# Performance work log

Measured on AMD Instinct MI355X. Metric: run time of the kernel, lower is better.

## Reference

```python
import jax, jax.numpy as jnp
import numpy as np

EPS = 1e-5


def _gcn_norm(edge_index, N):
    # symmetric GCN normalization with self-loops: D^-1/2 (A+I) D^-1/2
    row, col = edge_index[0], edge_index[1]
    loop = jnp.arange(N, dtype=row.dtype)
    row_f = jnp.concatenate([row, loop])
    col_f = jnp.concatenate([col, loop])
    deg = jax.ops.segment_sum(jnp.ones_like(row_f, dtype=jnp.float32), row_f, num_segments=N)
    dinv = jnp.where(deg > 0, jax.lax.rsqrt(jnp.maximum(deg, 1.0)), 0.0)
    norm = dinv[row_f] * dinv[col_f]  # [E+N]
    return row_f, col_f, norm


def _gcn_conv(h, W, b, row_f, col_f, norm, N):
    h = h @ W  # [N, C_out] small GEMM
    msg = h[col_f] * norm[:, None]  # gather over edges  [E+N, C_out]
    return jax.ops.segment_sum(msg, row_f, num_segments=N) + b


def _bn_eval(h, gamma, beta, mean, var):
    return (h - mean) * jax.lax.rsqrt(var + EPS) * gamma + beta


def setup_inputs() -> dict:
    key = jax.random.key(0)
    ks = jax.random.split(key, 12)
    N, E = 100000, 1600000
    C_in, C_hid, C_out = 64, 64, 64
    x = jax.random.normal(ks[0], (N, C_in), dtype=jnp.float32)
    edge_index = jax.random.randint(ks[1], (2, E), 0, N, dtype=jnp.int32)
    s = 1.0 / np.sqrt(C_hid)
    inp = {
        "x": x,
        "edge_index": edge_index,
        "W1": jax.random.normal(ks[2], (C_in, C_hid), dtype=jnp.float32) * s,
        "b1": jnp.zeros((C_hid,), jnp.float32),
        "g1": jnp.ones((C_hid,), jnp.float32),
        "be1": jnp.zeros((C_hid,), jnp.float32),
        "m1": jax.random.normal(ks[3], (C_hid,), dtype=jnp.float32) * 0.1,
        "v1": jax.random.uniform(ks[4], (C_hid,), minval=0.5, maxval=1.5, dtype=jnp.float32),
        "W2": jax.random.normal(ks[5], (C_hid, C_hid), dtype=jnp.float32) * s,
        "b2": jnp.zeros((C_hid,), jnp.float32),
        "g2": jnp.ones((C_hid,), jnp.float32),
        "be2": jnp.zeros((C_hid,), jnp.float32),
        "m2": jax.random.normal(ks[6], (C_hid,), dtype=jnp.float32) * 0.1,
        "v2": jax.random.uniform(ks[7], (C_hid,), minval=0.5, maxval=1.5, dtype=jnp.float32),
        "W3": jax.random.normal(ks[8], (C_hid, C_out), dtype=jnp.float32) * s,
        "b3": jnp.zeros((C_out,), jnp.float32),
    }
    return inp


def reference(x, edge_index, W1, b1, g1, be1, m1, v1, W2, b2, g2, be2, m2, v2, W3, b3):
    N = x.shape[0]
    row_f, col_f, norm = _gcn_norm(edge_index, N)  # cached=True: computed once
    h = _gcn_conv(x, W1, b1, row_f, col_f, norm, N)
    h = jax.nn.relu(_bn_eval(h, g1, be1, m1, v1))  # dropout off (eval)
    h = _gcn_conv(h, W2, b2, row_f, col_f, norm, N)
    h = jax.nn.relu(_bn_eval(h, g2, be2, m2, v2))
    global_embeddings = h
    hc_predictions = _gcn_conv(global_embeddings, W3, b3, row_f, col_f, norm, N)
    return (global_embeddings, hc_predictions)
```

## Files before the change

kernel.cpp:

```cpp
#include <hip/hip_runtime.h>

typedef __attribute__((ext_vector_type(8))) short bfrag8;
typedef __attribute__((ext_vector_type(4))) float facc4;
typedef __attribute__((ext_vector_type(8))) unsigned short u16x8;

#define CROWS  256
#define NCBMAX 512
#define CAP    8192
#define CHUNK  4096
#define SLACK  772
#define BPITCH (CAP + SLACK)

static __device__ __forceinline__ float bf2f(ushort u) {
    union { unsigned int i; float f; } x;
    x.i = ((unsigned int)u) << 16;
    return x.f;
}
static __device__ __forceinline__ ushort f2bf(float f) {
    union { float f; unsigned int i; } x;
    x.f = f;
    unsigned int r = x.i + 0x7FFFu + ((x.i >> 16) & 1u);
    return (ushort)(r >> 16);
}


__global__ void k_cinit(int* __restrict__ ccur, int ncb,
                        ushort* __restrict__ ta, ushort* __restrict__ tb, int N) {
    int b = blockIdx.x * blockDim.x + threadIdx.x;
    if (b < ncb) ccur[b] = b * CAP;
    if (blockIdx.x == 0 && threadIdx.x < 64) {
        ta[(size_t)N * 64 + threadIdx.x] = 0;
        tb[(size_t)N * 64 + threadIdx.x] = 0;
    }
}

__global__ void k_part(const int* __restrict__ row, const int* __restrict__ col, int E,
                       int* __restrict__ ccur, int* __restrict__ bkt, int ncb) {
    __shared__ int recs[CHUNK];
    __shared__ unsigned short cbl[CHUNK];
    __shared__ int hist[NCBMAX], lbase[NCBMAX], loff[NCBMAX];
    int tid = threadIdx.x;
    int chunk0 = blockIdx.x * CHUNK;
    for (int i = tid; i < ncb; i += blockDim.x) hist[i] = 0;
    __syncthreads();
    for (int j = tid; j < CHUNK; j += blockDim.x) {
        int e = chunk0 + j;
        if (e < E) {
            int r = row[e];
            int cb = r >> 8;
            recs[j] = ((r & (CROWS - 1)) << 17) | col[e];
            cbl[j] = (unsigned short)cb;
            atomicAdd(&hist[cb], 1);
        } else cbl[j] = 0xFFFF;
    }
    __syncthreads();
    for (int i = tid; i < ncb; i += blockDim.x) {
        int h = hist[i];
        lbase[i] = h ? atomicAdd(&ccur[i], h) : 0;
        loff[i] = 0;
    }
    __syncthreads();
    for (int j = tid; j < CHUNK; j += blockDim.x) {
        unsigned short cb = cbl[j];
        if (cb != 0xFFFF) {
            int p = lbase[cb] + atomicAdd(&loff[cb], 1);
            if (p < (cb + 1) * CAP) bkt[p] = recs[j];
        }
    }
}

__global__ void k_build(const int* __restrict__ bkt, const int* __restrict__ ccur,
                        int* __restrict__ rptr, int* __restrict__ deg,
                        float* __restrict__ dinv, int* __restrict__ cidx, int N) {
    __shared__ int hist[CROWS], wstart[CROWS], cur[CROWS], psum[CROWS];
    int tid = threadIdx.x;
    int b = blockIdx.x;
    int lo = b * CROWS;
    int nr = min(CROWS, N - lo);
    int in0 = b * CAP;
    int cntE = min(ccur[b] - in0, CAP);
    int out0 = b * BPITCH;

    if (tid < CROWS) hist[tid] = 0;
    __syncthreads();
    for (int i = tid; i < cntE; i += blockDim.x)
        atomicAdd(&hist[bkt[in0 + i] >> 17], 1);
    __syncthreads();
    int d = 0, ep = 0;
    if (tid < CROWS) {
        d = hist[tid];
        ep = (d + 3) & ~3;
        psum[tid] = ep;
    }
    __syncthreads();
    #pragma unroll
    for (int off = 1; off < CROWS; off <<= 1) {
        int t = (tid >= off && tid < CROWS) ? psum[tid - off] : 0;
        __syncthreads();
        if (tid < CROWS) psum[tid] += t;
        __syncthreads();
    }
    if (tid < CROWS) {
        int ws = out0 + psum[tid] - ep;
        wstart[tid] = ws;
        cur[tid] = ws;
        if (tid < nr) {
            rptr[lo + tid] = ws;
            deg[lo + tid] = d;
            dinv[lo + tid] = rsqrtf((float)(d + 1));
        }
    }
    __syncthreads();
    for (int i = tid; i < cntE; i += blockDim.x) {
        int v = bkt[in0 + i];
        int p = atomicAdd(&cur[v >> 17], 1);
        cidx[p] = v & 0x1FFFF;
    }
    __syncthreads();
    if (tid < nr)
        for (int j = d; j < ep; j++) cidx[wstart[tid] + j] = N;
}

template <bool FP32IN>
__global__ void k_gemm(const void* __restrict__ Hv, const float* __restrict__ W,
                       const float* __restrict__ dinv,
                       ushort* __restrict__ T, int ntiles, int N) {
    int lane = threadIdx.x & 63;
    int wid = (blockIdx.x * blockDim.x + threadIdx.x) >> 6;
    int nw = (gridDim.x * blockDim.x) >> 6;
    int m = lane & 15, quad = lane >> 4;

    bfrag8 bf[2][4];
    #pragma unroll
    for (int s = 0; s < 2; s++)
        #pragma unroll
        for (int c = 0; c < 4; c++) {
            bfrag8 f;
            #pragma unroll
            for (int j = 0; j < 8; j++) {
                int k = 32 * s + quad * 8 + j;
                f[j] = (short)f2bf(W[k * 64 + 16 * c + m]);
            }
            bf[s][c] = f;
        }

    for (int t = wid; t < ntiles; t += nw) {
        int nodeA = t * 16 + m;
        if (nodeA >= N) nodeA = N - 1;
        bfrag8 a0, a1;
        if (FP32IN) {
            const float* arow = (const float*)Hv + (size_t)nodeA * 64;
            #pragma unroll
            for (int s = 0; s < 2; s++) {
                float4 u0 = *(const float4*)(arow + s * 32 + quad * 8);
                float4 u1 = *(const float4*)(arow + s * 32 + quad * 8 + 4);
                bfrag8 f;
                f[0] = (short)f2bf(u0.x); f[1] = (short)f2bf(u0.y);
                f[2] = (short)f2bf(u0.z); f[3] = (short)f2bf(u0.w);
                f[4] = (short)f2bf(u1.x); f[5] = (short)f2bf(u1.y);
                f[6] = (short)f2bf(u1.z); f[7] = (short)f2bf(u1.w);
                if (s == 0) a0 = f; else a1 = f;
            }
        } else {
            const ushort* arow = (const ushort*)Hv + (size_t)nodeA * 64;
            a0 = *(const bfrag8*)(arow + quad * 8);
            a1 = *(const bfrag8*)(arow + 32 + quad * 8);
        }
        facc4 acc[4];
        #pragma unroll
        for (int c = 0; c < 4; c++) { acc[c][0]=0.f; acc[c][1]=0.f; acc[c][2]=0.f; acc[c][3]=0.f; }
        #pragma unroll
        for (int c = 0; c < 4; c++) {
            acc[c] = __builtin_amdgcn_mfma_f32_16x16x32_bf16(a0, bf[0][c], acc[c], 0, 0, 0);
            acc[c] = __builtin_amdgcn_mfma_f32_16x16x32_bf16(a1, bf[1][c], acc[c], 0, 0, 0);
        }
        #pragma unroll
        for (int c = 0; c < 4; c++)
            #pragma unroll
            for (int r = 0; r < 4; r++) {
                int node = t * 16 + quad * 4 + r;
                if (node < N)
                    T[(size_t)node * 64 + c * 16 + m] = f2bf(dinv[node] * acc[c][r]);
            }
    }
}

template <bool FUSE>
__global__ void k_aggf(const ushort* __restrict__ T2, const int* __restrict__ rptr,
                       const int* __restrict__ deg, const float* __restrict__ dinv,
                       const int* __restrict__ cidx,
                       const float* __restrict__ bias, const float* __restrict__ g,
                       const float* __restrict__ be, const float* __restrict__ mm,
                       const float* __restrict__ vv, int do_bn,
                       const float* __restrict__ Wn,
                       float* __restrict__ outf, ushort* __restrict__ Tn, int N) {
    __shared__ ushort lds_h[32][72];

    int tid = threadIdx.x;
    int lane = tid & 63;
    int wl = tid >> 6;
    int grp = lane >> 3;
    int s = lane & 7;
    int loc = wl * 8 + grp;
    int r = blockIdx.x * 32 + loc;
    bool rv = (r < N);

    float bb[8], sc[8], sh[8];
    #pragma unroll
    for (int k = 0; k < 8; k++) { bb[k] = bias[s * 8 + k]; sc[k] = 1.f; sh[k] = 0.f; }
    if (do_bn) {
        #pragma unroll
        for (int k = 0; k < 8; k++) {
            sc[k] = g[s * 8 + k] * rsqrtf(vv[s * 8 + k] + 1e-5f);
            sh[k] = be[s * 8 + k] - mm[s * 8 + k] * sc[k];
        }
    }

    int start = rv ? rptr[r] : 0;
    int ep = rv ? ((deg[r] + 3) & ~3) : 0;
    float a[8];
    #pragma unroll
    for (int k = 0; k < 8; k++) a[k] = 0.f;
    int i = 0;
    for (; i + 8 <= ep; i += 8) {
        int4 c4 = *(const int4*)(cidx + start + i);
        int4 d4 = *(const int4*)(cidx + start + i + 4);
        u16x8 t0 = *(const u16x8*)(T2 + (size_t)c4.x * 64 + s * 8);
        u16x8 t1 = *(const u16x8*)(T2 + (size_t)c4.y * 64 + s * 8);
        u16x8 t2 = *(const u16x8*)(T2 + (size_t)c4.z * 64 + s * 8);
        u16x8 t3 = *(const u16x8*)(T2 + (size_t)c4.w * 64 + s * 8);
        u16x8 t4 = *(const u16x8*)(T2 + (size_t)d4.x * 64 + s * 8);
        u16x8 t5 = *(const u16x8*)(T2 + (size_t)d4.y * 64 + s * 8);
        u16x8 t6 = *(const u16x8*)(T2 + (size_t)d4.z * 64 + s * 8);
        u16x8 t7 = *(const u16x8*)(T2 + (size_t)d4.w * 64 + s * 8);
        #pragma unroll
        for (int k = 0; k < 8; k++)
            a[k] += ((bf2f(t0[k]) + bf2f(t1[k])) + (bf2f(t2[k]) + bf2f(t3[k]))) +
                    ((bf2f(t4[k]) + bf2f(t5[k])) + (bf2f(t6[k]) + bf2f(t7[k])));
    }
    if (i < ep) {
        int4 c4 = *(const int4*)(cidx + start + i);
        u16x8 t0 = *(const u16x8*)(T2 + (size_t)c4.x * 64 + s * 8);
        u16x8 t1 = *(const u16x8*)(T2 + (size_t)c4.y * 64 + s * 8);
        u16x8 t2 = *(const u16x8*)(T2 + (size_t)c4.z * 64 + s * 8);
        u16x8 t3 = *(const u16x8*)(T2 + (size_t)c4.w * 64 + s * 8);
        #pragma unroll
        for (int k = 0; k < 8; k++)
            a[k] += (bf2f(t0[k]) + bf2f(t1[k])) + (bf2f(t2[k]) + bf2f(t3[k]));
    }

    float v[8];
    #pragma unroll
    for (int k = 0; k < 8; k++) v[k] = 0.f;
    if (rv) {
        u16x8 sf = *(const u16x8*)(T2 + (size_t)r * 64 + s * 8);
        float dr = dinv[r];
        #pragma unroll
        for (int k = 0; k < 8; k++) {
            v[k] = dr * (a[k] + bf2f(sf[k])) + bb[k];
            if (do_bn) v[k] = fmaxf(v[k] * sc[k] + sh[k], 0.f);
        }
        if (outf) {
            *(float4*)(outf + (size_t)r * 64 + s * 8) = make_float4(v[0], v[1], v[2], v[3]);
            *(float4*)(outf + (size_t)r * 64 + s * 8 + 4) = make_float4(v[4], v[5], v[6], v[7]);
        }
    }

    if constexpr (FUSE) {
        u16x8 hv;
        #pragma unroll
        for (int k = 0; k < 8; k++) hv[k] = rv ? f2bf(v[k]) : (ushort)0;
        *(u16x8*)&lds_h[loc][s * 8] = hv;

        int m = lane & 15, quad = lane >> 4;
        int rtile = wl >> 1, chalf = wl & 1;
        bfrag8 bw[2][2];
        #pragma unroll
        for (int ks = 0; ks < 2; ks++)
            #pragma unroll
            for (int c = 0; c < 2; c++) {
                bfrag8 f;
                #pragma unroll
                for (int j = 0; j < 8; j++) {
                    int k = 32 * ks + quad * 8 + j;
                    f[j] = (short)f2bf(Wn[k * 64 + chalf * 32 + c * 16 + m]);
                }
                bw[ks][c] = f;
            }
        __syncthreads();

        bfrag8 a0 = *(const bfrag8*)&lds_h[rtile * 16 + m][quad * 8];
        bfrag8 a1 = *(const bfrag8*)&lds_h[rtile * 16 + m][32 + quad * 8];
        facc4 acc[2];
        #pragma unroll
        for (int c = 0; c < 2; c++) { acc[c][0]=0.f; acc[c][1]=0.f; acc[c][2]=0.f; acc[c][3]=0.f; }
        #pragma unroll
        for (int c = 0; c < 2; c++) {
            acc[c] = __builtin_amdgcn_mfma_f32_16x16x32_bf16(a0, bw[0][c], acc[c], 0, 0, 0);
            acc[c] = __builtin_amdgcn_mfma_f32_16x16x32_bf16(a1, bw[1][c], acc[c], 0, 0, 0);
        }
        int nodeBase = blockIdx.x * 32 + rtile * 16;
        #pragma unroll
        for (int c = 0; c < 2; c++)
            #pragma unroll
            for (int rr = 0; rr < 4; rr++) {
                int node = nodeBase + quad * 4 + rr;
                if (node < N)
                    Tn[(size_t)node * 64 + chalf * 32 + c * 16 + m] =
                        f2bf(dinv[node] * acc[c][rr]);
            }
    }
}


extern "C" void kernel_launch(void* const* d_in, const int* in_sizes, int n_in,
                              void* d_out, int out_size, void* d_ws, size_t ws_size,
                              hipStream_t stream) {
    const float* x  = (const float*)d_in[0];
    const int*   ei = (const int*)d_in[1];
    const float *W1 = (const float*)d_in[2],  *b1 = (const float*)d_in[3];
    const float *g1 = (const float*)d_in[4],  *be1= (const float*)d_in[5];
    const float *m1 = (const float*)d_in[6],  *v1 = (const float*)d_in[7];
    const float *W2 = (const float*)d_in[8],  *b2 = (const float*)d_in[9];
    const float *g2 = (const float*)d_in[10], *be2= (const float*)d_in[11];
    const float *m2 = (const float*)d_in[12], *v2 = (const float*)d_in[13];
    const float *W3 = (const float*)d_in[14], *b3 = (const float*)d_in[15];

    int N = in_sizes[0] / 64;
    int E = in_sizes[1] / 2;
    const int* row = ei;
    const int* col = ei + E;
    int ncb = (N + CROWS - 1) / CROWS;

    char* p = (char*)d_ws;
    auto take = [&](size_t b) -> char* {
        char* q = p;
        p += (b + 255) & ~(size_t)255;
        return q;
    };
    int*    ccur  = (int*)   take((size_t)ncb * 4);
    int*    rptr  = (int*)   take((size_t)N * 4);
    int*    deg   = (int*)   take((size_t)N * 4);
    float*  dinv  = (float*) take((size_t)N * 4);
    int*    bkt   = (int*)   take((size_t)ncb * CAP * 4);
    int*    cidx  = (int*)   take((size_t)ncb * BPITCH * 4 + 1024);
    ushort* ta    = (ushort*)take((size_t)(N + 1) * 64 * 2);
    ushort* tb    = (ushort*)take((size_t)(N + 1) * 64 * 2);

    const int TB = 256;
    const int TBP = 1024;
    int nchunks = (E + CHUNK - 1) / CHUNK;
    k_cinit<<<(ncb + TB - 1) / TB, TB, 0, stream>>>(ccur, ncb, ta, tb, N);
    k_part <<<nchunks, TBP, 0, stream>>>(row, col, E, ccur, bkt, ncb);
    k_build<<<ncb, TBP, 0, stream>>>(bkt, ccur, rptr, deg, dinv, cidx, N);

    float* outp = (float*)d_out;
    int ntiles = (N + 15) >> 4;
    int GG = (ntiles + 3) / 4;
    int GA = (N + 31) / 32;

    k_gemm<true><<<GG, TB, 0, stream>>>(x, W1, dinv, ta, ntiles, N);
    k_aggf<true><<<GA, TB, 0, stream>>>(ta, rptr, deg, dinv, cidx, b1, g1, be1, m1, v1, 1,
                                        W2, (float*)nullptr, tb, N);
    k_aggf<true><<<GA, TB, 0, stream>>>(tb, rptr, deg, dinv, cidx, b2, g2, be2, m2, v2, 1,
                                        W3, outp, ta, N);
    k_aggf<false><<<GA, TB, 0, stream>>>(ta, rptr, deg, dinv, cidx, b3, b3, b3, b3, b3, 0,
                                         (const float*)nullptr,
                                         outp + (size_t)N * 64, (ushort*)nullptr, N);
}
```

Before: 272.1 us.

## Sort CSR neighbors by column tile and prepack weights and BN params

The CSR build now histograms edges per (row, column-tile) sub-bucket, so each row's neighbor list is grouped by source-node range. The aim is better cache locality during the gather in the aggregation kernels. A new prep kernel converts the three weight matrices once into a bf16 MFMA-fragment layout and folds bias plus batch-norm into one scale and shift per channel, so every block no longer repeats the strided float-to-bf16 weight loads and rsqrt. The cost is larger LDS histograms in k_build and one extra small kernel launch.

```diff
diff --git a/kernel.cpp b/kernel.cpp
--- a/kernel.cpp
+++ b/kernel.cpp
@@ -10,6 +10,8 @@
 #define CHUNK  4096
 #define SLACK  772
 #define BPITCH (CAP + SLACK)
+#define TSH    14
+#define NTMAX  8
 
 static __device__ __forceinline__ float bf2f(ushort u) {
     union { unsigned int i; float f; } x;
@@ -21,6 +23,41 @@
     x.f = f;
     unsigned int r = x.i + 0x7FFFu + ((x.i >> 16) & 1u);
     return (ushort)(r >> 16);
+}
+
+__global__ void k_prep(const float* __restrict__ W1, const float* __restrict__ W2,
+                       const float* __restrict__ W3,
+                       const float* __restrict__ b1, const float* __restrict__ g1,
+                       const float* __restrict__ be1, const float* __restrict__ m1,
+                       const float* __restrict__ v1,
+                       const float* __restrict__ b2, const float* __restrict__ g2,
+                       const float* __restrict__ be2, const float* __restrict__ m2,
+                       const float* __restrict__ v2,
+                       const float* __restrict__ b3,
+                       ushort* __restrict__ wp, float* __restrict__ pp) {
+    int l = blockIdx.x;
+    const float* W = (l == 0) ? W1 : (l == 1) ? W2 : W3;
+    ushort* wo = wp + l * 4096;
+    for (int idx = threadIdx.x; idx < 4096; idx += blockDim.x) {
+        int j = idx & 7, m = (idx >> 3) & 15, quad = (idx >> 7) & 3;
+        int ks = (idx >> 9) & 1, c2 = idx >> 10;
+        wo[idx] = f2bf(W[(32 * ks + 8 * quad + j) * 64 + c2 * 16 + m]);
+    }
+    if (threadIdx.x < 64) {
+        int ch = threadIdx.x;
+        float PS, PH;
+        if (l == 0) {
+            float sc = g1[ch] * rsqrtf(v1[ch] + 1e-5f);
+            PS = sc; PH = be1[ch] - m1[ch] * sc + b1[ch] * sc;
+        } else if (l == 1) {
+            float sc = g2[ch] * rsqrtf(v2[ch] + 1e-5f);
+            PS = sc; PH = be2[ch] - m2[ch] * sc + b2[ch] * sc;
+        } else {
+            PS = 1.f; PH = b3[ch];
+        }
+        pp[l * 128 + ch] = PS;
+        pp[l * 128 + 64 + ch] = PH;
+    }
 }
 
 
@@ -72,7 +109,9 @@
 __global__ void k_build(const int* __restrict__ bkt, const int* __restrict__ ccur,
                         int* __restrict__ rptr, int* __restrict__ deg,
                         float* __restrict__ dinv, int* __restrict__ cidx, int N) {
-    __shared__ int hist[CROWS], wstart[CROWS], cur[CROWS], psum[CROWS];
+    __shared__ int hist4[CROWS * NTMAX];
+    __shared__ int cur4[CROWS * NTMAX];
+    __shared__ int wstart[CROWS], psum[CROWS], degs[CROWS];
     int tid = threadIdx.x;
     int b = blockIdx.x;
     int lo = b * CROWS;
@@ -81,16 +120,20 @@
     int cntE = min(ccur[b] - in0, CAP);
     int out0 = b * BPITCH;
 
-    if (tid < CROWS) hist[tid] = 0;
-    __syncthreads();
-    for (int i = tid; i < cntE; i += blockDim.x)
-        atomicAdd(&hist[bkt[in0 + i] >> 17], 1);
+    for (int i = tid; i < CROWS * NTMAX; i += blockDim.x) hist4[i] = 0;
+    __syncthreads();
+    for (int i = tid; i < cntE; i += blockDim.x) {
+        int v = bkt[in0 + i];
+        atomicAdd(&hist4[(v >> 17) * NTMAX + ((v & 0x1FFFF) >> TSH)], 1);
+    }
     __syncthreads();
     int d = 0, ep = 0;
     if (tid < CROWS) {
-        d = hist[tid];
+        #pragma unroll
+        for (int t = 0; t < NTMAX; t++) d += hist4[tid * NTMAX + t];
         ep = (d + 3) & ~3;
         psum[tid] = ep;
+        degs[tid] = d;
     }
     __syncthreads();
     #pragma unroll
@@ -103,7 +146,12 @@
     if (tid < CROWS) {
         int ws = out0 + psum[tid] - ep;
         wstart[tid] = ws;
-        cur[tid] = ws;
+        int off = ws;
+        #pragma unroll
+        for (int t = 0; t < NTMAX; t++) {
+            cur4[tid * NTMAX + t] = off;
+            off += hist4[tid * NTMAX + t];
+        }
         if (tid < nr) {
             rptr[lo + tid] = ws;
             deg[lo + tid] = d;
@@ -113,16 +161,19 @@
     __syncthreads();
     for (int i = tid; i < cntE; i += blockDim.x) {
         int v = bkt[in0 + i];
-        int p = atomicAdd(&cur[v >> 17], 1);
-        cidx[p] = v & 0x1FFFF;
-    }
-    __syncthreads();
-    if (tid < nr)
-        for (int j = d; j < ep; j++) cidx[wstart[tid] + j] = N;
-}
-
-template <bool FP32IN>
-__global__ void k_gemm(const void* __restrict__ Hv, const float* __restrict__ W,
+        int c = v & 0x1FFFF;
+        int p = atomicAdd(&cur4[(v >> 17) * NTMAX + (c >> TSH)], 1);
+        cidx[p] = c;
+    }
+    __syncthreads();
+    if (tid < nr) {
+        int dd = degs[tid];
+        int epp = (dd + 3) & ~3;
+        for (int j = dd; j < epp; j++) cidx[wstart[tid] + j] = N;
+    }
+}
+
+__global__ void k_gemm(const float* __restrict__ Hv, const ushort* __restrict__ wq,
                        const float* __restrict__ dinv,
                        ushort* __restrict__ T, int ntiles, int N) {
     int lane = threadIdx.x & 63;
@@ -134,37 +185,25 @@
     #pragma unroll
     for (int s = 0; s < 2; s++)
         #pragma unroll
-        for (int c = 0; c < 4; c++) {
-            bfrag8 f;
-            #pragma unroll
-            for (int j = 0; j < 8; j++) {
-                int k = 32 * s + quad * 8 + j;
-                f[j] = (short)f2bf(W[k * 64 + 16 * c + m]);
-            }
-            bf[s][c] = f;
-        }
+        for (int c = 0; c < 4; c++)
+            bf[s][c] = *(const bfrag8*)(wq +
+                (size_t)((((c * 2 + s) * 4 + quad) * 16 + m) * 8));
 
     for (int t = wid; t < ntiles; t += nw) {
         int nodeA = t * 16 + m;
         if (nodeA >= N) nodeA = N - 1;
         bfrag8 a0, a1;
-        if (FP32IN) {
-            const float* arow = (const float*)Hv + (size_t)nodeA * 64;
-            #pragma unroll
-            for (int s = 0; s < 2; s++) {
-                float4 u0 = *(const float4*)(arow + s * 32 + quad * 8);
-                float4 u1 = *(const float4*)(arow + s * 32 + quad * 8 + 4);
-                bfrag8 f;
-                f[0] = (short)f2bf(u0.x); f[1] = (short)f2bf(u0.y);
-                f[2] = (short)f2bf(u0.z); f[3] = (short)f2bf(u0.w);
-                f[4] = (short)f2bf(u1.x); f[5] = (short)f2bf(u1.y);
-                f[6] = (short)f2bf(u1.z); f[7] = (short)f2bf(u1.w);
-                if (s == 0) a0 = f; else a1 = f;
-            }
-        } else {
-            const ushort* arow = (const ushort*)Hv + (size_t)nodeA * 64;
-            a0 = *(const bfrag8*)(arow + quad * 8);
-            a1 = *(const bfrag8*)(arow + 32 + quad * 8);
+        const float* arow = Hv + (size_t)nodeA * 64;
+        #pragma unroll
+        for (int s = 0; s < 2; s++) {
+            float4 u0 = *(const float4*)(arow + s * 32 + quad * 8);
+            float4 u1 = *(const float4*)(arow + s * 32 + quad * 8 + 4);
+            bfrag8 f;
+            f[0] = (short)f2bf(u0.x); f[1] = (short)f2bf(u0.y);
+            f[2] = (short)f2bf(u0.z); f[3] = (short)f2bf(u0.w);
+            f[4] = (short)f2bf(u1.x); f[5] = (short)f2bf(u1.y);
+            f[6] = (short)f2bf(u1.z); f[7] = (short)f2bf(u1.w);
+            if (s == 0) a0 = f; else a1 = f;
         }
         facc4 acc[4];
         #pragma unroll
@@ -189,10 +228,8 @@
 __global__ void k_aggf(const ushort* __restrict__ T2, const int* __restrict__ rptr,
                        const int* __restrict__ deg, const float* __restrict__ dinv,
                        const int* __restrict__ cidx,
-                       const float* __restrict__ bias, const float* __restrict__ g,
-                       const float* __restrict__ be, const float* __restrict__ mm,
-                       const float* __restrict__ vv, int do_bn,
-                       const float* __restrict__ Wn,
+                       const float* __restrict__ pp, int relu,
+                       const ushort* __restrict__ wq,
                        float* __restrict__ outf, ushort* __restrict__ Tn, int N) {
     __shared__ ushort lds_h[32][72];
 
@@ -204,17 +241,6 @@
     int loc = wl * 8 + grp;
     int r = blockIdx.x * 32 + loc;
     bool rv = (r < N);
-
-    float bb[8], sc[8], sh[8];
-    #pragma unroll
-    for (int k = 0; k < 8; k++) { bb[k] = bias[s * 8 + k]; sc[k] = 1.f; sh[k] = 0.f; }
-    if (do_bn) {
-        #pragma unroll
-        for (int k = 0; k < 8; k++) {
-            sc[k] = g[s * 8 + k] * rsqrtf(vv[s * 8 + k] + 1e-5f);
-            sh[k] = be[s * 8 + k] - mm[s * 8 + k] * sc[k];
-        }
-    }
 
     int start = rv ? rptr[r] : 0;
     int ep = rv ? ((deg[r] + 3) & ~3) : 0;
@@ -249,6 +275,13 @@
             a[k] += (bf2f(t0[k]) + bf2f(t1[k])) + (bf2f(t2[k]) + bf2f(t3[k]));
     }
 
+    float4 ps0 = *(const float4*)(pp + s * 8);
+    float4 ps1 = *(const float4*)(pp + s * 8 + 4);
+    float4 ph0 = *(const float4*)(pp + 64 + s * 8);
+    float4 ph1 = *(const float4*)(pp + 64 + s * 8 + 4);
+    float PS[8] = {ps0.x, ps0.y, ps0.z, ps0.w, ps1.x, ps1.y, ps1.z, ps1.w};
+    float PH[8] = {ph0.x, ph0.y, ph0.z, ph0.w, ph1.x, ph1.y, ph1.z, ph1.w};
+
     float v[8];
     #pragma unroll
     for (int k = 0; k < 8; k++) v[k] = 0.f;
@@ -257,8 +290,8 @@
         float dr = dinv[r];
         #pragma unroll
         for (int k = 0; k < 8; k++) {
-            v[k] = dr * (a[k] + bf2f(sf[k])) + bb[k];
-            if (do_bn) v[k] = fmaxf(v[k] * sc[k] + sh[k], 0.f);
+            v[k] = dr * (a[k] + bf2f(sf[k])) * PS[k] + PH[k];
+            if (relu) v[k] = fmaxf(v[k], 0.f);
         }
         if (outf) {
             *(float4*)(outf + (size_t)r * 64 + s * 8) = make_float4(v[0], v[1], v[2], v[3]);
@@ -278,15 +311,9 @@
         #pragma unroll
         for (int ks = 0; ks < 2; ks++)
             #pragma unroll
-            for (int c = 0; c < 2; c++) {
-                bfrag8 f;
-                #pragma unroll
-                for (int j = 0; j < 8; j++) {
-                    int k = 32 * ks + quad * 8 + j;
-                    f[j] = (short)f2bf(Wn[k * 64 + chalf * 32 + c * 16 + m]);
-                }
-                bw[ks][c] = f;
-            }
+            for (int c = 0; c < 2; c++)
+                bw[ks][c] = *(const bfrag8*)(wq +
+                    (size_t)(((((chalf * 2 + c) * 2 + ks) * 4 + quad) * 16 + m) * 8));
         __syncthreads();
 
         bfrag8 a0 = *(const bfrag8*)&lds_h[rtile * 16 + m][quad * 8];
@@ -306,7 +333,7 @@
             for (int rr = 0; rr < 4; rr++) {
                 int node = nodeBase + quad * 4 + rr;
                 if (node < N)
-                    Tn[(size_t)node * 64 + chalf * 32 + c * 16 + m] =
+                    Tn[(size_t)node * 64 + (chalf * 2 + c) * 16 + m] =
                         f2bf(dinv[node] * acc[c][rr]);
             }
     }
@@ -342,6 +369,8 @@
     int*    rptr  = (int*)   take((size_t)N * 4);
     int*    deg   = (int*)   take((size_t)N * 4);
     float*  dinv  = (float*) take((size_t)N * 4);
+    ushort* wp    = (ushort*)take((size_t)3 * 4096 * 2);
+    float*  pp    = (float*) take((size_t)3 * 128 * 4);
     int*    bkt   = (int*)   take((size_t)ncb * CAP * 4);
     int*    cidx  = (int*)   take((size_t)ncb * BPITCH * 4 + 1024);
     ushort* ta    = (ushort*)take((size_t)(N + 1) * 64 * 2);
@@ -350,6 +379,8 @@
     const int TB = 256;
     const int TBP = 1024;
     int nchunks = (E + CHUNK - 1) / CHUNK;
+    k_prep <<<3, TB, 0, stream>>>(W1, W2, W3, b1, g1, be1, m1, v1,
+                                  b2, g2, be2, m2, v2, b3, wp, pp);
     k_cinit<<<(ncb + TB - 1) / TB, TB, 0, stream>>>(ccur, ncb, ta, tb, N);
     k_part <<<nchunks, TBP, 0, stream>>>(row, col, E, ccur, bkt, ncb);
     k_build<<<ncb, TBP, 0, stream>>>(bkt, ccur, rptr, deg, dinv, cidx, N);
@@ -359,12 +390,12 @@
     int GG = (ntiles + 3) / 4;
     int GA = (N + 31) / 32;
 
-    k_gemm<true><<<GG, TB, 0, stream>>>(x, W1, dinv, ta, ntiles, N);
-    k_aggf<true><<<GA, TB, 0, stream>>>(ta, rptr, deg, dinv, cidx, b1, g1, be1, m1, v1, 1,
-                                        W2, (float*)nullptr, tb, N);
-    k_aggf<true><<<GA, TB, 0, stream>>>(tb, rptr, deg, dinv, cidx, b2, g2, be2, m2, v2, 1,
-                                        W3, outp, ta, N);
-    k_aggf<false><<<GA, TB, 0, stream>>>(ta, rptr, deg, dinv, cidx, b3, b3, b3, b3, b3, 0,
-                                         (const float*)nullptr,
+    k_gemm<<<GG, TB, 0, stream>>>(x, wp, dinv, ta, ntiles, N);
+    k_aggf<true><<<GA, TB, 0, stream>>>(ta, rptr, deg, dinv, cidx, pp, 1,
+                                        wp + 4096, (float*)nullptr, tb, N);
+    k_aggf<true><<<GA, TB, 0, stream>>>(tb, rptr, deg, dinv, cidx, pp + 128, 1,
+                                        wp + 8192, outp, ta, N);
+    k_aggf<false><<<GA, TB, 0, stream>>>(ta, rptr, deg, dinv, cidx, pp + 256, 0,
+                                         (const ushort*)nullptr,
                                          outp + (size_t)N * 64, (ushort*)nullptr, N);
 }
```

Measured after the change: 261.2 us. 4.0% less time.
